# Performance work log

Measured on AMD Instinct MI355X. Metric: run time of the kernel, lower is better.

Reference implementation:

```python
import jax, jax.numpy as jnp
import numpy as np

DIM = 768
HEADS = 12
HEAD_DIM = DIM // HEADS
SCALE = HEAD_DIM ** -0.5


def setup_inputs() -> dict:
    key = jax.random.key(0)
    k1, k2, k3, k4 = jax.random.split(key, 4)
    x = jax.random.normal(k1, (1, 4096, DIM), dtype=jnp.float32)
    # qkv: Linear(dim, 3*dim), bias=False
    W_qkv = jax.random.normal(k2, (DIM, 3 * DIM), dtype=jnp.float32) * (DIM ** -0.5)
    # proj: Linear(dim, dim) with bias
    W_proj = jax.random.normal(k3, (DIM, DIM), dtype=jnp.float32) * (DIM ** -0.5)
    b_proj = jax.random.normal(k4, (DIM,), dtype=jnp.float32) * 0.01
    return {"x": x, "W_qkv": W_qkv, "W_proj": W_proj, "b_proj": b_proj}


def reference(x, W_qkv, W_proj, b_proj):
    b, n, d = x.shape
    qkv = x @ W_qkv                                  # [b, n, 3d]
    q, k, v = jnp.split(qkv, 3, axis=-1)             # each [b, n, d]
    # split heads: [b, n, (h hd)] -> [b, h, n, hd]
    def heads(t):
        return t.reshape(b, n, HEADS, HEAD_DIM).transpose(0, 2, 1, 3)
    q, k, v = heads(q) * SCALE, heads(k), heads(v)
    sim = jnp.einsum('bhid,bhjd->bhij', q, k)        # [b, h, n, n] -- full score matrix
    attn = jax.nn.softmax(sim, axis=-1)
    out = jnp.einsum('bhij,bhjd->bhid', attn, v)     # [b, h, n, hd]
    out = out.transpose(0, 2, 1, 3).reshape(b, n, d)  # merge heads
    return out @ W_proj + b_proj
```

## Files before the change

kernel.cpp:

```cpp
#include <hip/hip_runtime.h>
#include <math.h>

#define TOKENS 4096
#define DMODEL 768
#define NHEADS 12
#define HDIM   64
#define QKV_N  2304
#define ATTN_SCALE 0.125f
#define QSCALE_LOG2E (0.125f * 1.44269504088896340736f)

typedef __attribute__((ext_vector_type(8))) short bf16x8;
typedef __attribute__((ext_vector_type(4))) float floatx4;

__device__ __forceinline__ ushort f2bf(float f) {
    union { float f; unsigned u; } cv; cv.f = f;
    unsigned u = cv.u;
    u += 0x7fffu + ((u >> 16) & 1u);
    return (ushort)(u >> 16);
}

__device__ __forceinline__ unsigned cvt_pk_bf16(float a, float b) {
    unsigned r;
    asm("v_cvt_pk_bf16_f32 %0, %1, %2" : "=v"(r) : "v"(a), "v"(b));
    return r;
}

__device__ __forceinline__ void gl2lds16(const ushort* g, ushort* l) {
    __builtin_amdgcn_global_load_lds(
        (const __attribute__((address_space(1))) void*)g,
        (__attribute__((address_space(3))) void*)l, 16, 0, 0);
}

__device__ __forceinline__ bf16x8 frag(const ushort* ls, int row, int chunk) {
    return *(const bf16x8*)(ls + row * 64 + ((chunk ^ (row & 7)) * 8));
}

__global__ __launch_bounds__(256) void cvt_bf16_kernel(
    const float* __restrict__ in, ushort* __restrict__ out, int n4)
{
    const int i = blockIdx.x * 256 + threadIdx.x;
    if (i < n4) {
        const float4 v = ((const float4*)in)[i];
        ushort4 h;
        h.x = f2bf(v.x); h.y = f2bf(v.y); h.z = f2bf(v.z); h.w = f2bf(v.w);
        ((ushort4*)out)[i] = h;
    }
}

__global__ __launch_bounds__(256) void transpose_cvt_kernel(
    const float* __restrict__ in, ushort* __restrict__ out, int R, int C)
{
    __shared__ ushort tile[32][33];
    const int tx  = threadIdx.x & 31;
    const int ty8 = threadIdx.x >> 5;
    const int c0 = blockIdx.x * 32;
    const int r0 = blockIdx.y * 32;
    #pragma unroll
    for (int p = 0; p < 4; ++p) {
        const int r = ty8 + p * 8;
        tile[r][tx] = f2bf(in[(size_t)(r0 + r) * C + c0 + tx]);
    }
    __syncthreads();
    #pragma unroll
    for (int p = 0; p < 4; ++p) {
        const int c = ty8 + p * 8;
        out[(size_t)(c0 + c) * R + r0 + tx] = tile[tx][c];
    }
}

template<int NT>
__device__ __forceinline__ void gemm_body_async(
    const ushort* __restrict__ A, const ushort* __restrict__ Bt, int K,
    int m0, int n0, floatx4 acc[4][NT], ushort* ls)
{
    ushort* lsA = ls;
    ushort* lsB = ls + 8192;

    const int tid  = threadIdx.x;
    const int lane = tid & 63;
    const int wave = tid >> 6;
    const int wm = wave >> 1, wn = wave & 1;
    const int quad = lane >> 4, l16 = lane & 15;

    const int lrow = lane >> 3;
    const int csw  = ((lane & 7) ^ lrow) * 8;

    const ushort* gA = A  + (size_t)(m0 + wave * 32 + lrow) * K + csw;
    const ushort* gB = Bt + (size_t)(n0 + wave * NT * 8 + lrow) * K + csw;
    ushort* lA = lsA + (wave * 32) * 64;
    ushort* lB = lsB + (wave * NT * 8) * 64;

    for (int k0 = 0; k0 < K; k0 += 64) {
        __syncthreads();
        #pragma unroll
        for (int p = 0; p < 4; ++p)
            gl2lds16(gA + (size_t)p * 8 * K + k0, lA + p * 8 * 64);
        #pragma unroll
        for (int p = 0; p < NT; ++p)
            gl2lds16(gB + (size_t)p * 8 * K + k0, lB + p * 8 * 64);
        __syncthreads();

        #pragma unroll
        for (int ks = 0; ks < 2; ++ks) {
            bf16x8 af[4], bfr[NT];
            #pragma unroll
            for (int mt = 0; mt < 4; ++mt)
                af[mt] = frag(lsA, wm * 64 + mt * 16 + l16, ks * 4 + quad);
            #pragma unroll
            for (int nt = 0; nt < NT; ++nt)
                bfr[nt] = frag(lsB, wn * NT * 16 + nt * 16 + l16, ks * 4 + quad);
            #pragma unroll
            for (int mt = 0; mt < 4; ++mt)
                #pragma unroll
                for (int nt = 0; nt < NT; ++nt)
                    acc[mt][nt] = __builtin_amdgcn_mfma_f32_16x16x32_bf16(
                        af[mt], bfr[nt], acc[mt][nt], 0, 0, 0);
        }
    }
}

__global__ __launch_bounds__(256) void gemm_qkv_mfma(
    const ushort* __restrict__ Xb, const ushort* __restrict__ Wt,
    ushort* __restrict__ Qb, ushort* __restrict__ Kb, ushort* __restrict__ Vt)
{
    __shared__ __align__(16) ushort ls[16384];
    const int m0 = blockIdx.y * 128;
    const int n0 = blockIdx.x * 128;

    floatx4 acc[4][4] = {};
    gemm_body_async<4>(Xb, Wt, DMODEL, m0, n0, acc, ls);

    const int tid  = threadIdx.x;
    const int lane = tid & 63;
    const int wave = tid >> 6;
    const int wm = wave >> 1, wn = wave & 1;
    const int quad = lane >> 4, l16 = lane & 15;

    if (n0 < 2 * DMODEL) {
        const float scale = (n0 < DMODEL) ? QSCALE_LOG2E : 1.0f;
        ushort* outp = (n0 < DMODEL) ? Qb : Kb;
        const int colg = (n0 < DMODEL) ? n0 : n0 - DMODEL;
        #pragma unroll
        for (int p = 0; p < 2; ++p) {
            __syncthreads();
            if (wm == p) {
                #pragma unroll
                for (int mt = 0; mt < 4; ++mt)
                    #pragma unroll
                    for (int nt = 0; nt < 4; ++nt) {
                        const int row = mt * 16 + quad * 4;
                        const int col = wn * 64 + nt * 16 + l16;
                        #pragma unroll
                        for (int r = 0; r < 4; ++r)
                            ls[(row + r) * 136 + col] = f2bf(acc[mt][nt][r] * scale);
                    }
            }
            __syncthreads();
            #pragma unroll
            for (int p2 = 0; p2 < 4; ++p2) {
                const int row = (tid >> 4) + p2 * 16;
                const int c8  = (tid & 15) * 8;
                *(uint4*)(outp + (size_t)(m0 + p * 64 + row) * DMODEL + colg + c8) =
                    *(const uint4*)(ls + row * 136 + c8);
            }
        }
    } else {
        const int hd0 = n0 - 2 * DMODEL;
        #pragma unroll
        for (int p = 0; p < 2; ++p) {
            __syncthreads();
            if (wn == p) {
                #pragma unroll
                for (int mt = 0; mt < 4; ++mt)
                    #pragma unroll
                    for (int nt = 0; nt < 4; ++nt) {
                        const int hd  = nt * 16 + l16;
                        const int tok = wm * 64 + mt * 16 + quad * 4;
                        #pragma unroll
                        for (int r = 0; r < 4; ++r)
                            ls[hd * 136 + tok + r] = f2bf(acc[mt][nt][r]);
                    }
            }
            __syncthreads();
            #pragma unroll
            for (int p2 = 0; p2 < 4; ++p2) {
                const int row = (tid >> 4) + p2 * 16;
                const int c8  = (tid & 15) * 8;
                *(uint4*)(Vt + (size_t)(hd0 + p * 64 + row) * TOKENS + m0 + c8) =
                    *(const uint4*)(ls + row * 136 + c8);
            }
        }
    }
}

__global__ __launch_bounds__(256) void gemm_proj_mfma(
    const ushort* __restrict__ Ab, const ushort* __restrict__ Wt,
    const float* __restrict__ bias, float* __restrict__ out)
{
    __shared__ __align__(16) ushort ls[12288];
    const int m0 = blockIdx.y * 128;
    const int n0 = blockIdx.x * 64;

    floatx4 acc[4][2] = {};
    gemm_body_async<2>(Ab, Wt, DMODEL, m0, n0, acc, ls);

    const int lane = threadIdx.x & 63;
    const int wave = threadIdx.x >> 6;
    const int wm = wave >> 1, wn = wave & 1;
    const int quad = lane >> 4, l16 = lane & 15;
    const int row0 = m0 + wm * 64 + quad * 4;
    const int col0 = n0 + wn * 32;

    #pragma unroll
    for (int nt = 0; nt < 2; ++nt) {
        const int col = col0 + nt * 16 + l16;
        const float bv = bias[col];
        #pragma unroll
        for (int mt = 0; mt < 4; ++mt)
            #pragma unroll
            for (int r = 0; r < 4; ++r)
                out[(size_t)(row0 + mt * 16 + r) * DMODEL + col] =
                    acc[mt][nt][r] + bv;
    }
}

__global__ __launch_bounds__(256, 3) void attn_mfma_kernel(
    const ushort* __restrict__ Qb, const ushort* __restrict__ Kb,
    const ushort* __restrict__ Vt, ushort* __restrict__ attn_out)
{
    __shared__ __align__(16) ushort lds[25728];

    const int tid  = threadIdx.x;
    const int wave = tid >> 6;
    const int lane = tid & 63;
    const int quad = lane >> 4;
    const int l16  = lane & 15;

    const int lin = blockIdx.x + blockIdx.y * 64;
    const int wsw = (lin & 7) * 96 + (lin >> 3);
    const int h   = wsw >> 6;
    const int i0  = (wsw & 63) * 64;

    bf16x8 qf[4][2];
    #pragma unroll
    for (int jt = 0; jt < 4; ++jt) {
        const ushort* qb = Qb + (size_t)(i0 + jt * 16 + l16) * DMODEL + h * HDIM;
        qf[jt][0] = *(const bf16x8*)(qb + quad * 8);
        qf[jt][1] = *(const bf16x8*)(qb + 32 + quad * 8);
    }

    bf16x8 ones;
    #pragma unroll
    for (int i = 0; i < 8; ++i) ones[i] = (short)0x3F80;

    floatx4 O[4][4] = {};
    floatx4 Ol[4]   = {};

    ushort* wls = lds + wave * 6144;

    const int lrow8 = lane >> 3;
    const int csw8  = ((lane & 7) ^ lrow8) * 8;
    const ushort* gK0 = Kb + (size_t)(wave * 16 + lrow8) * DMODEL + h * HDIM + csw8;
    const ushort* gK1 = gK0 + (size_t)8 * DMODEL;

    const ushort* gV0 = Vt + (size_t)(h * HDIM + (lane >> 1)) * TOKENS
                           + wave * 16 + (((lane & 1) ^ ((lane >> 3) & 1)) * 8);
    const ushort* gV1 = gV0 + (size_t)32 * TOKENS;

    const int vo = ((quad >> 1) ^ ((l16 >> 2) & 1)) * 8 + (quad & 1) * 4;

    union { bf16x8 v; unsigned u[4]; } pa[4];

    gl2lds16(gK0, wls);
    gl2lds16(gK1, wls + 512);
    gl2lds16(gV0, wls + 2048);
    gl2lds16(gV1, wls + 2048 + 512);

    for (int u = 0; u < 32; ++u) {
        const int s0 = (u & 1) << 1;
        ushort* Kc0 = wls;
        ushort* Kc1 = wls + 1024;
        ushort* V0  = wls + 2048 + s0 * 1024;
        ushort* V1  = wls + 2048 + (s0 + 1) * 1024;
        ushort* Vn  = wls + 2048 + ((s0 + 2) & 3) * 1024;

        {
            const size_t t1 = (size_t)(2 * u + 1) * 64;
            gl2lds16(gK0 + t1 * DMODEL, Kc1);
            gl2lds16(gK1 + t1 * DMODEL, Kc1 + 512);
            gl2lds16(gV0 + t1, V1);
            gl2lds16(gV1 + t1, V1 + 512);
        }
        asm volatile("s_waitcnt vmcnt(4)" ::: "memory");
        __builtin_amdgcn_sched_barrier(0);

        {
            const bf16x8 a0 = frag(Kc0, l16, quad);
            const bf16x8 a1 = frag(Kc0, l16, 4 + quad);
            __builtin_amdgcn_s_setprio(1);
            #pragma unroll
            for (int jt = 0; jt < 4; ++jt) {
                floatx4 s = {0.f, 0.f, 0.f, 0.f};
                s = __builtin_amdgcn_mfma_f32_16x16x32_bf16(a0, qf[jt][0], s, 0, 0, 0);
                s = __builtin_amdgcn_mfma_f32_16x16x32_bf16(a1, qf[jt][1], s, 0, 0, 0);
                pa[jt].u[0] = cvt_pk_bf16(__builtin_amdgcn_exp2f(s[0]),
                                          __builtin_amdgcn_exp2f(s[1]));
                pa[jt].u[1] = cvt_pk_bf16(__builtin_amdgcn_exp2f(s[2]),
                                          __builtin_amdgcn_exp2f(s[3]));
            }
            __builtin_amdgcn_s_setprio(0);
        }

        if (u < 31) {
            const size_t t2 = (size_t)(2 * u + 2) * 64;
            gl2lds16(gK0 + t2 * DMODEL, Kc0);
            gl2lds16(gK1 + t2 * DMODEL, Kc0 + 512);
            gl2lds16(gV0 + t2, Vn);
            gl2lds16(gV1 + t2, Vn + 512);
            asm volatile("s_waitcnt vmcnt(4)" ::: "memory");
        } else {
            asm volatile("s_waitcnt vmcnt(0)" ::: "memory");
        }
        __builtin_amdgcn_sched_barrier(0);

        {
            const bf16x8 a0 = frag(Kc1, l16, quad);
            const bf16x8 a1 = frag(Kc1, l16, 4 + quad);
            __builtin_amdgcn_s_setprio(1);
            #pragma unroll
            for (int jt = 0; jt < 4; ++jt) {
                floatx4 s = {0.f, 0.f, 0.f, 0.f};
                s = __builtin_amdgcn_mfma_f32_16x16x32_bf16(a0, qf[jt][0], s, 0, 0, 0);
                s = __builtin_amdgcn_mfma_f32_16x16x32_bf16(a1, qf[jt][1], s, 0, 0, 0);
                pa[jt].u[2] = cvt_pk_bf16(__builtin_amdgcn_exp2f(s[0]),
                                          __builtin_amdgcn_exp2f(s[1]));
                pa[jt].u[3] = cvt_pk_bf16(__builtin_amdgcn_exp2f(s[2]),
                                          __builtin_amdgcn_exp2f(s[3]));
            }
            __builtin_amdgcn_s_setprio(0);
        }

        __builtin_amdgcn_s_setprio(1);
        #pragma unroll
        for (int nt = 0; nt < 4; ++nt) {
            const int ro = (nt * 16 + l16) * 16 + vo;
            union { bf16x8 v; uint2 d[2]; } vu;
            vu.d[0] = *(const uint2*)(V0 + ro);
            vu.d[1] = *(const uint2*)(V1 + ro);
            #pragma unroll
            for (int jt = 0; jt < 4; ++jt)
                O[jt][nt] = __builtin_amdgcn_mfma_f32_16x16x32_bf16(
                    pa[jt].v, vu.v, O[jt][nt], 0, 0, 0);
        }
        #pragma unroll
        for (int jt = 0; jt < 4; ++jt)
            Ol[jt] = __builtin_amdgcn_mfma_f32_16x16x32_bf16(
                pa[jt].v, ones, Ol[jt], 0, 0, 0);
        __builtin_amdgcn_s_setprio(0);
    }

    __syncthreads();
    float* Of  = (float*)lds;
    float* Olf = ((float*)lds) + 3 * 64 * 66;
    if (wave != 0) {
        const int rg = (wave - 1) * 64 * 66;
        #pragma unroll
        for (int jt = 0; jt < 4; ++jt) {
            #pragma unroll
            for (int nt = 0; nt < 4; ++nt)
                #pragma unroll
                for (int r = 0; r < 4; ++r)
                    Of[rg + (jt * 16 + quad * 4 + r) * 66 + nt * 16 + l16] = O[jt][nt][r];
            if (l16 == 0) {
                #pragma unroll
                for (int r = 0; r < 4; ++r)
                    Olf[(wave - 1) * 64 + jt * 16 + quad * 4 + r] = Ol[jt][r];
            }
        }
    }
    __syncthreads();
    if (wave == 0) {
        #pragma unroll
        for (int jt = 0; jt < 4; ++jt) {
            const int qr = jt * 16 + quad * 4;
            float linv[4];
            #pragma unroll
            for (int r = 0; r < 4; ++r) {
                const float l = Ol[jt][r] + Olf[qr + r] + Olf[64 + qr + r]
                              + Olf[128 + qr + r];
                linv[r] = __builtin_amdgcn_rcpf(l);
            }
            #pragma unroll
            for (int nt = 0; nt < 4; ++nt) {
                const int d = h * HDIM + nt * 16 + l16;
                #pragma unroll
                for (int r = 0; r < 4; ++r) {
                    const float o = O[jt][nt][r]
                        + Of[(qr + r) * 66 + nt * 16 + l16]
                        + Of[64 * 66 + (qr + r) * 66 + nt * 16 + l16]
                        + Of[2 * 64 * 66 + (qr + r) * 66 + nt * 16 + l16];
                    attn_out[(size_t)(i0 + qr + r) * DMODEL + d] = f2bf(o * linv[r]);
                }
            }
        }
    }
}

extern "C" void kernel_launch(void* const* d_in, const int* in_sizes, int n_in,
                              void* d_out, int out_size, void* d_ws, size_t ws_size,
                              hipStream_t stream)
{
    const float* x     = (const float*)d_in[0];
    const float* Wqkv  = (const float*)d_in[1];
    const float* Wproj = (const float*)d_in[2];
    const float* bproj = (const float*)d_in[3];
    float* out = (float*)d_out;

    ushort* Xb     = (ushort*)d_ws;
    ushort* WqkvT  = Xb    + (size_t)TOKENS * DMODEL;
    ushort* WprojT = WqkvT + (size_t)QKV_N * DMODEL;
    ushort* Qb     = WprojT + (size_t)DMODEL * DMODEL;
    ushort* Kb     = Qb    + (size_t)TOKENS * DMODEL;
    ushort* Vt     = Kb    + (size_t)TOKENS * DMODEL;
    ushort* attn   = Vt    + (size_t)TOKENS * DMODEL;

    cvt_bf16_kernel<<<dim3(TOKENS * DMODEL / 4 / 256), 256, 0, stream>>>(
        x, Xb, TOKENS * DMODEL / 4);
    transpose_cvt_kernel<<<dim3(QKV_N / 32, DMODEL / 32), 256, 0, stream>>>(
        Wqkv, WqkvT, DMODEL, QKV_N);
    transpose_cvt_kernel<<<dim3(DMODEL / 32, DMODEL / 32), 256, 0, stream>>>(
        Wproj, WprojT, DMODEL, DMODEL);

    gemm_qkv_mfma<<<dim3(QKV_N / 128, TOKENS / 128), 256, 0, stream>>>(
        Xb, WqkvT, Qb, Kb, Vt);

    attn_mfma_kernel<<<dim3(TOKENS / 64, NHEADS), 256, 0, stream>>>(
        Qb, Kb, Vt, attn);

    gemm_proj_mfma<<<dim3(DMODEL / 64, TOKENS / 128), 256, 0, stream>>>(
        attn, WprojT, bproj, out);
}
```

Before: 203.1 us.

## Fuse input conversion kernels and remap GEMM block order across XCDs

Merges the x conversion and the two weight transpose-convert kernels into one prep kernel that dispatches on block index, which removes two kernel launches. Both GEMMs also remap the linear block id so that blocks that are consecutive in the (lin & 7) chiplet round-robin get contiguous tiles. The intent is better L2 locality per XCD on MI355X. The remap assumes the grid size is divisible by 8 and adds some divide and modulo arithmetic per block.

```diff
diff --git a/kernel.cpp b/kernel.cpp
--- a/kernel.cpp
+++ b/kernel.cpp
@@ -35,26 +35,39 @@
     return *(const bf16x8*)(ls + row * 64 + ((chunk ^ (row & 7)) * 8));
 }
 
-__global__ __launch_bounds__(256) void cvt_bf16_kernel(
-    const float* __restrict__ in, ushort* __restrict__ out, int n4)
-{
-    const int i = blockIdx.x * 256 + threadIdx.x;
-    if (i < n4) {
-        const float4 v = ((const float4*)in)[i];
+__global__ __launch_bounds__(256) void prep_kernel(
+    const float* __restrict__ x, const float* __restrict__ Wqkv,
+    const float* __restrict__ Wproj, ushort* __restrict__ Xb,
+    ushort* __restrict__ WqkvT, ushort* __restrict__ WprojT)
+{
+    __shared__ ushort tile[32][33];
+    const int bid = blockIdx.x;
+    const int tid = threadIdx.x;
+
+    if (bid < 3072) {
+        const int i = bid * 256 + tid;
+        const float4 v = ((const float4*)x)[i];
         ushort4 h;
         h.x = f2bf(v.x); h.y = f2bf(v.y); h.z = f2bf(v.z); h.w = f2bf(v.w);
-        ((ushort4*)out)[i] = h;
-    }
-}
-
-__global__ __launch_bounds__(256) void transpose_cvt_kernel(
-    const float* __restrict__ in, ushort* __restrict__ out, int R, int C)
-{
-    __shared__ ushort tile[32][33];
-    const int tx  = threadIdx.x & 31;
-    const int ty8 = threadIdx.x >> 5;
-    const int c0 = blockIdx.x * 32;
-    const int r0 = blockIdx.y * 32;
+        ((ushort4*)Xb)[i] = h;
+        return;
+    }
+
+    const float* in; ushort* out; int C, bx, by;
+    if (bid < 3072 + 1728) {
+        const int b = bid - 3072;
+        in = Wqkv; out = WqkvT; C = QKV_N;
+        bx = b % 72; by = b / 72;
+    } else {
+        const int b = bid - 4800;
+        in = Wproj; out = WprojT; C = DMODEL;
+        bx = b % 24; by = b / 24;
+    }
+    const int R  = DMODEL;
+    const int tx = tid & 31;
+    const int ty8 = tid >> 5;
+    const int c0 = bx * 32;
+    const int r0 = by * 32;
     #pragma unroll
     for (int p = 0; p < 4; ++p) {
         const int r = ty8 + p * 8;
@@ -124,8 +137,10 @@
     ushort* __restrict__ Qb, ushort* __restrict__ Kb, ushort* __restrict__ Vt)
 {
     __shared__ __align__(16) ushort ls[16384];
-    const int m0 = blockIdx.y * 128;
-    const int n0 = blockIdx.x * 128;
+    const int lin = blockIdx.x + blockIdx.y * 18;
+    const int w   = (lin & 7) * 72 + (lin >> 3);
+    const int m0  = (w / 18) * 128;
+    const int n0  = (w % 18) * 128;
 
     floatx4 acc[4][4] = {};
     gemm_body_async<4>(Xb, Wt, DMODEL, m0, n0, acc, ls);
@@ -198,8 +213,10 @@
     const float* __restrict__ bias, float* __restrict__ out)
 {
     __shared__ __align__(16) ushort ls[12288];
-    const int m0 = blockIdx.y * 128;
-    const int n0 = blockIdx.x * 64;
+    const int lin = blockIdx.x + blockIdx.y * 12;
+    const int w   = (lin & 7) * 48 + (lin >> 3);
+    const int m0  = (w / 12) * 128;
+    const int n0  = (w % 12) * 64;
 
     floatx4 acc[4][2] = {};
     gemm_body_async<2>(Ab, Wt, DMODEL, m0, n0, acc, ls);
@@ -424,12 +441,8 @@
     ushort* Vt     = Kb    + (size_t)TOKENS * DMODEL;
     ushort* attn   = Vt    + (size_t)TOKENS * DMODEL;
 
-    cvt_bf16_kernel<<<dim3(TOKENS * DMODEL / 4 / 256), 256, 0, stream>>>(
-        x, Xb, TOKENS * DMODEL / 4);
-    transpose_cvt_kernel<<<dim3(QKV_N / 32, DMODEL / 32), 256, 0, stream>>>(
-        Wqkv, WqkvT, DMODEL, QKV_N);
-    transpose_cvt_kernel<<<dim3(DMODEL / 32, DMODEL / 32), 256, 0, stream>>>(
-        Wproj, WprojT, DMODEL, DMODEL);
+    prep_kernel<<<dim3(5376), 256, 0, stream>>>(
+        x, Wqkv, Wproj, Xb, WqkvT, WprojT);
 
     gemm_qkv_mfma<<<dim3(QKV_N / 128, TOKENS / 128), 256, 0, stream>>>(
         Xb, WqkvT, Qb, Kb, Vt);
```

Result: faster. 196.3 us (-3.3%).
